# Performance work log

Hardware: AMD Instinct MI355X
Metric: run time of the kernel (lower is better)

Reference implementation:

```python
import jax, jax.numpy as jnp
import numpy as np

B, L, C = 2, 2048, 1024
H, DK = 16, 64  # multiNum, dk
EPS = 1e-5
MASK_VAL = -2**15 + 1  # matches masked_fill value in torch source


def layer_norm(x, g, b):
    mu = jnp.mean(x, axis=-1, keepdims=True)
    var = jnp.var(x, axis=-1, keepdims=True)
    return (x - mu) * jax.lax.rsqrt(var + EPS) * g + b


def setup_inputs() -> dict:
    key = jax.random.key(0)
    ks = jax.random.split(key, 12)
    s_in = 1.0 / np.sqrt(C)
    s_attn = 1.0 / np.sqrt(H * DK)
    return {
        "qx": jax.random.normal(ks[0], (B, L, C), jnp.float32),
        "kx": jax.random.normal(ks[1], (B, L, C), jnp.float32),
        "vx": jax.random.normal(ks[2], (B, L, C), jnp.float32),
        "maskPAD": jax.random.randint(ks[3], (B, L, L), 0, 2, jnp.int32),
        "ln_g": jnp.ones((C,), jnp.float32),
        "ln_b": jnp.zeros((C,), jnp.float32),
        "wq": jax.random.uniform(ks[4], (C, H * DK), jnp.float32, -s_in, s_in),
        "bq": jax.random.uniform(ks[5], (H * DK,), jnp.float32, -s_in, s_in),
        "wk": jax.random.uniform(ks[6], (C, H * DK), jnp.float32, -s_in, s_in),
        "bk": jax.random.uniform(ks[7], (H * DK,), jnp.float32, -s_in, s_in),
        "wv": jax.random.uniform(ks[8], (C, H * DK), jnp.float32, -s_in, s_in),
        "bv": jax.random.uniform(ks[9], (H * DK,), jnp.float32, -s_in, s_in),
        "wo": jax.random.uniform(ks[10], (H * DK, C), jnp.float32, -s_attn, s_attn),
        "bo": jax.random.uniform(ks[11], (C,), jnp.float32, -s_attn, s_attn),
    }


def reference(qx, kx, vx, maskPAD, ln_g, ln_b, wq, bq, wk, bk, wv, bv, wo, bo):
    # PreLN with shared LayerNorm params across q/k/v (as in source)
    qn = layer_norm(qx, ln_g, ln_b)
    kn = layer_norm(kx, ln_g, ln_b)
    vn = layer_norm(vx, ln_g, ln_b)
    # project and split heads: [B, H, L, DK]
    q = (qn @ wq + bq).reshape(B, L, H, DK).transpose(0, 2, 1, 3)
    k = (kn @ wk + bk).reshape(B, L, H, DK).transpose(0, 2, 1, 3)
    v = (vn @ wv + bv).reshape(B, L, H, DK).transpose(0, 2, 1, 3)
    scores = jnp.einsum("bhqd,bhkd->bhqk", q, k) / np.sqrt(DK).astype(np.float32)
    scores = jnp.where((maskPAD == 0)[:, None, :, :], jnp.float32(MASK_VAL), scores)
    alpha = jax.nn.softmax(scores, axis=-1)
    z = jnp.einsum("bhqk,bhkd->bhqd", alpha, v)
    z = z.transpose(0, 2, 1, 3).reshape(B, L, H * DK)
    return z @ wo + bo
```

## Files before the change

### kernel.cpp

```cpp
#include <hip/hip_runtime.h>
#include <hip/hip_bf16.h>

#define B_ 2
#define L_ 2048
#define C_ 1024
#define H_ 16
#define DK_ 64
#define M_ (B_*L_)
#define MASK_VALF (-32767.0f)
#define LOG2E 1.44269504088896f

typedef __attribute__((ext_vector_type(8))) short bf16x8;
typedef __attribute__((ext_vector_type(4))) float f32x4;
typedef __attribute__((ext_vector_type(4))) unsigned uint4v;

static __device__ __forceinline__ short f2bf(float f) {
    __hip_bfloat16 h = __float2bfloat16(f);
    return *reinterpret_cast<short*>(&h);
}

static __device__ __forceinline__ float exp2_raw(float x) {
    float r;
    asm("v_exp_f32 %0, %1" : "=v"(r) : "v"(x));
    return r;
}
static __device__ __forceinline__ unsigned cvt_pk_bf16(float lo, float hi) {
    unsigned r;
    asm("v_cvt_pk_bf16_f32 %0, %1, %2" : "=v"(r) : "v"(lo), "v"(hi));
    return r;
}

__global__ __launch_bounds__(256) void prep_kernel(
    const float* __restrict__ qx, const float* __restrict__ kx, const float* __restrict__ vx,
    const float* __restrict__ g, const float* __restrict__ bias,
    short* __restrict__ qn, short* __restrict__ kn, short* __restrict__ vn,
    const float* __restrict__ wq, const float* __restrict__ wk,
    const float* __restrict__ wv, const float* __restrict__ wo,
    short* __restrict__ wqt, short* __restrict__ wkt,
    short* __restrict__ wvt, short* __restrict__ wot,
    const int* __restrict__ mask, unsigned long long* __restrict__ bits)
{
    const int bid = blockIdx.x;
    const int t = threadIdx.x;

    if (bid < 3*M_) {
        const int row = bid & (M_ - 1);
        const int which = bid >> 12;
        const float* src = (which == 0) ? qx : (which == 1) ? kx : vx;
        short* dst = (which == 0) ? qn : (which == 1) ? kn : vn;
        src += (size_t)row * C_;
        dst += (size_t)row * C_;
        float4 xv = reinterpret_cast<const float4*>(src)[t];
        float s  = xv.x + xv.y + xv.z + xv.w;
        float s2 = xv.x*xv.x + xv.y*xv.y + xv.z*xv.z + xv.w*xv.w;
        #pragma unroll
        for (int off = 32; off > 0; off >>= 1) {
            s  += __shfl_down(s, off);
            s2 += __shfl_down(s2, off);
        }
        __shared__ float red[8];
        const int wid = t >> 6, lane = t & 63;
        if (lane == 0) { red[wid] = s; red[4 + wid] = s2; }
        __syncthreads();
        const float ts  = red[0] + red[1] + red[2] + red[3];
        const float ts2 = red[4] + red[5] + red[6] + red[7];
        const float mu  = ts * (1.0f / C_);
        const float var = ts2 * (1.0f / C_) - mu * mu;
        const float rs  = rsqrtf(var + 1e-5f);
        float4 gv = reinterpret_cast<const float4*>(g)[t];
        float4 bv = reinterpret_cast<const float4*>(bias)[t];
        short4 o;
        o.x = f2bf((xv.x - mu) * rs * gv.x + bv.x);
        o.y = f2bf((xv.y - mu) * rs * gv.y + bv.y);
        o.z = f2bf((xv.z - mu) * rs * gv.z + bv.z);
        o.w = f2bf((xv.w - mu) * rs * gv.w + bv.w);
        reinterpret_cast<short4*>(dst)[t] = o;
    } else if (bid < 3*M_ + 4096) {
        const int b2 = bid - 3*M_;
        const int mz = b2 >> 10;
        const int bx = b2 & 31, by = (b2 >> 5) & 31;
        const float* w = (mz==0)?wq:(mz==1)?wk:(mz==2)?wv:wo;
        short* wt = (mz==0)?wqt:(mz==1)?wkt:(mz==2)?wvt:wot;
        __shared__ float tile[32][33];
        const int tx = t & 31, ty = t >> 5;
        const int k0 = bx * 32, n0 = by * 32;
        #pragma unroll
        for (int r = 0; r < 4; r++) {
            const int k = k0 + ty + r*8;
            tile[ty + r*8][tx] = w[(size_t)k * 1024 + n0 + tx];
        }
        __syncthreads();
        #pragma unroll
        for (int r = 0; r < 4; r++) {
            const int n = n0 + ty + r*8;
            wt[(size_t)n * 1024 + k0 + tx] = f2bf(tile[tx][ty + r*8]);
        }
    } else {
        const int b3 = bid - (3*M_ + 4096);
        const int gw = b3 * 4 + (t >> 6);
        const int lane = t & 63;
        const int k = (gw & 31) * 64 + lane;
        const int rowq = gw >> 5;
        const int v = mask[(size_t)rowq * L_ + k];
        unsigned long long bal = __ballot(v != 0);
        if (lane == 0) bits[gw] = bal;
    }
}

__device__ __forceinline__ void gemm_core_128(
    const short* __restrict__ Abf, const short* __restrict__ Bt,
    int m0, int n0, short* lds, f32x4 (&acc)[4][4])
{
    const int t = threadIdx.x, w = t >> 6, l = t & 63;
    const int wm = w >> 1, wn = w & 1;
    const int l15 = l & 15, l4 = l >> 4;
    const int srow = t >> 2, scol = (t & 3) * 8;
    const short* aS = Abf + (size_t)(m0 + srow) * 1024 + scol;
    const short* bS = Bt  + (size_t)(n0 + srow) * 1024 + scol;
    char* lb = (char*)lds;
    const int wb = w * 1024;

    #define GSTAGE(buf, kt) do {                                                   \
        const int ko = (kt) * 32;                                                  \
        char* dst = lb + (buf)*16384;                                              \
        __builtin_amdgcn_global_load_lds(                                          \
            (const __attribute__((address_space(1))) void*)(aS + ko),              \
            (__attribute__((address_space(3))) void*)(dst + wb), 16, 0, 0);        \
        __builtin_amdgcn_global_load_lds(                                          \
            (const __attribute__((address_space(1))) void*)(aS + 64*1024 + ko),    \
            (__attribute__((address_space(3))) void*)(dst + wb + 4096), 16, 0, 0); \
        __builtin_amdgcn_global_load_lds(                                          \
            (const __attribute__((address_space(1))) void*)(bS + ko),              \
            (__attribute__((address_space(3))) void*)(dst + 8192 + wb), 16, 0, 0); \
        __builtin_amdgcn_global_load_lds(                                          \
            (const __attribute__((address_space(1))) void*)(bS + 64*1024 + ko),    \
            (__attribute__((address_space(3))) void*)(dst + 8192 + wb + 4096), 16, 0, 0); \
    } while (0)

    GSTAGE(0, 0);
    for (int kt = 0; kt < 32; ++kt) {
        __syncthreads();
        if (kt + 1 < 32) GSTAGE((kt + 1) & 1, kt + 1);
        const short* Lb = lds + (kt & 1) * 8192;
        bf16x8 af[4], bfr[4];
        #pragma unroll
        for (int fm = 0; fm < 4; fm++)
            af[fm] = *reinterpret_cast<const bf16x8*>(&Lb[(wm*64 + fm*16 + l15)*32 + l4*8]);
        #pragma unroll
        for (int fn = 0; fn < 4; fn++)
            bfr[fn] = *reinterpret_cast<const bf16x8*>(&Lb[4096 + (wn*64 + fn*16 + l15)*32 + l4*8]);
        #pragma unroll
        for (int fm = 0; fm < 4; fm++)
            #pragma unroll
            for (int fn = 0; fn < 4; fn++)
                acc[fm][fn] = __builtin_amdgcn_mfma_f32_16x16x32_bf16(af[fm], bfr[fn], acc[fm][fn], 0, 0, 0);
    }
    #undef GSTAGE
}

__global__ __launch_bounds__(256) void gemm_proj(
    const short* __restrict__ qn, const short* __restrict__ kn, const short* __restrict__ vn,
    const short* __restrict__ wqt, const short* __restrict__ wkt, const short* __restrict__ wvt,
    const float* __restrict__ bq, const float* __restrict__ bk, const float* __restrict__ bv,
    short* __restrict__ qb, short* __restrict__ kb, short* __restrict__ vtb)
{
    const int pi = blockIdx.y;
    const short* Abf = (pi==0)?qn:(pi==1)?kn:vn;
    const short* Bt  = (pi==0)?wqt:(pi==1)?wkt:wvt;
    const float* bias= (pi==0)?bq:(pi==1)?bk:bv;
    short* outp      = (pi==0)?qb:(pi==1)?kb:vtb;
    const float scale = (pi==0)?(0.125f*LOG2E):1.0f;

    __shared__ short lds[16384];
    const int bx0 = blockIdx.x;
    const int bx = (bx0 & 7) * 32 + (bx0 >> 3);
    const int m0 = (bx >> 3) * 128, n0 = (bx & 7) * 128;
    f32x4 acc[4][4] = {};
    gemm_core_128(Abf, Bt, m0, n0, lds, acc);

    const int t = threadIdx.x, w = t >> 6, l = t & 63;
    const int wm = w >> 1, wn = w & 1, l15 = l & 15, l4 = l >> 4;
    #pragma unroll
    for (int fn = 0; fn < 4; fn++) {
        const int col = n0 + wn*64 + fn*16 + l15;
        const float bsv = bias[col];
        const int h = col >> 6, dk = col & 63;
        #pragma unroll
        for (int fm = 0; fm < 4; fm++) {
            const int row0 = m0 + wm*64 + fm*16 + l4*4;
            const int bb = row0 >> 11, lr0 = row0 & (L_ - 1);
            if (pi == 2) {
                const int lrp = (lr0 & ~63) | ((fm >> 1)*32 + l4*8 + (fm & 1)*4);
                short4 s4;
                #pragma unroll
                for (int r = 0; r < 4; r++)
                    ((short*)&s4)[r] = f2bf(acc[fm][fn][r] + bsv);
                *reinterpret_cast<short4*>(
                    &outp[(((size_t)bb*H_ + h)*DK_ + dk)*L_ + lrp]) = s4;
            } else {
                #pragma unroll
                for (int r = 0; r < 4; r++) {
                    const float vvf = (acc[fm][fn][r] + bsv) * scale;
                    outp[(((size_t)bb*H_ + h)*L_ + lr0 + r)*DK_ + dk] = f2bf(vvf);
                }
            }
        }
    }
}

__global__ __launch_bounds__(256) void gemm_out_k(
    const short* __restrict__ zb, const short* __restrict__ wot,
    const float* __restrict__ bo, float* __restrict__ out)
{
    __shared__ short lds[12288];
    const int t = threadIdx.x, w = t >> 6, l = t & 63;
    const int wm = w >> 1, wn = w & 1;
    const int l15 = l & 15, l4 = l >> 4;
    const int bx0 = blockIdx.x;
    const int bx = (bx0 & 7) * 64 + (bx0 >> 3);
    const int m0 = (bx >> 3) * 64, n0 = (bx & 7) * 128;

    const int srow = l >> 2, scol = (l & 3) * 8;
    const short* aS = zb  + (size_t)(m0 + w*16 + srow) * 1024 + scol;
    const short* bS = wot + (size_t)(n0 + w*32 + srow) * 1024 + scol;
    char* lb = (char*)lds;

    f32x4 acc[2][4] = {};

    #define OSTAGE(buf, kt) do {                                                    \
        const int ko = (kt) * 32;                                                   \
        char* dst = lb + (buf)*12288;                                               \
        __builtin_amdgcn_global_load_lds(                                           \
            (const __attribute__((address_space(1))) void*)(aS + ko),               \
            (__attribute__((address_space(3))) void*)(dst + w*1024), 16, 0, 0);     \
        __builtin_amdgcn_global_load_lds(                                           \
            (const __attribute__((address_space(1))) void*)(bS + ko),               \
            (__attribute__((address_space(3))) void*)(dst + 4096 + w*2048), 16, 0, 0); \
        __builtin_amdgcn_global_load_lds(                                           \
            (const __attribute__((address_space(1))) void*)(bS + 16*1024 + ko),     \
            (__attribute__((address_space(3))) void*)(dst + 4096 + w*2048 + 1024), 16, 0, 0); \
    } while (0)

    OSTAGE(0, 0);
    for (int kt = 0; kt < 32; ++kt) {
        __syncthreads();
        if (kt + 1 < 32) OSTAGE((kt + 1) & 1, kt + 1);
        const short* Lb = lds + (kt & 1) * 6144;
        bf16x8 af[2], bfr[4];
        #pragma unroll
        for (int fm = 0; fm < 2; fm++)
            af[fm] = *reinterpret_cast<const bf16x8*>(&Lb[(wm*32 + fm*16 + l15)*32 + l4*8]);
        #pragma unroll
        for (int fn = 0; fn < 4; fn++)
            bfr[fn] = *reinterpret_cast<const bf16x8*>(&Lb[2048 + (wn*64 + fn*16 + l15)*32 + l4*8]);
        #pragma unroll
        for (int fm = 0; fm < 2; fm++)
            #pragma unroll
            for (int fn = 0; fn < 4; fn++)
                acc[fm][fn] = __builtin_amdgcn_mfma_f32_16x16x32_bf16(af[fm], bfr[fn], acc[fm][fn], 0, 0, 0);
    }
    #undef OSTAGE

    #pragma unroll
    for (int fn = 0; fn < 4; fn++) {
        const int col = n0 + wn*64 + fn*16 + l15;
        const float bsv = bo[col];
        #pragma unroll
        for (int fm = 0; fm < 2; fm++) {
            #pragma unroll
            for (int r = 0; r < 4; r++) {
                const int row = m0 + wm*32 + fm*16 + l4*4 + r;
                out[(size_t)row * C_ + col] = acc[fm][fn][r] + bsv;
            }
        }
    }
}

__global__ __launch_bounds__(512) void attn_kernel(
    const short* __restrict__ qbuf, const short* __restrict__ kbuf, const short* __restrict__ vt,
    const unsigned long long* __restrict__ mbits, short* __restrict__ zb)
{
    __shared__ char SM[65536];
    const int t = threadIdx.x, w = t >> 6, l = t & 63;
    const int l15 = l & 15, l4 = l >> 4;
    const int bid = blockIdx.x;
    const int bh = bid & 31, qb = bid >> 5;
    const int qt0 = qb * 128;
    const int b = bh >> 4, h = bh & 15;
    const size_t base  = (size_t)bh * L_ * DK_;
    const size_t vbase = (size_t)bh * DK_ * L_;

    const int q = qt0 + w*16 + l15;

    const int srow = w*8 + (l >> 3);
    const int scolb = ((l & 7) * 16) ^ ((srow & 7) << 4);

    const char* gkA = (const char*)(kbuf + base + (size_t)srow*DK_) + scolb;
    const char* gkB = gkA + 8192;
    const char* gvA = (const char*)(vt + vbase + (size_t)srow*L_) + scolb;
    const char* gvB = gvA + 128;

    char* kd0 = SM + w*1024;
    char* vd0 = SM + 8192 + w*1024;
    char* kd1 = SM + 16384 + w*1024;
    char* vd1 = SM + 16384 + 8192 + w*1024;

    const int sw = (l15 & 7) << 4;
    const char* pa = SM + l15*128 + ((l4*16) ^ sw);
    const char* pb = SM + l15*128 + ((64 + l4*16) ^ sw);

    bf16x8 qf[2];
    #pragma unroll
    for (int kk = 0; kk < 2; kk++)
        qf[kk] = *reinterpret_cast<const bf16x8*>(&qbuf[base + (size_t)q*DK_ + kk*32 + l4*8]);

    const uint2* mb32 = reinterpret_cast<const uint2*>(mbits + ((size_t)b*L_ + q) * (L_/64));

    f32x4 oacc[4];
    #pragma unroll
    for (int nt = 0; nt < 4; nt++) oacc[nt] = (f32x4){0.f, 0.f, 0.f, 0.f};
    f32x4 lacc = (f32x4){0.f, 0.f, 0.f, 0.f};

    uint4v onesu = {0x3F803F80u, 0x3F803F80u, 0x3F803F80u, 0x3F803F80u};
    const bf16x8 onesv = *reinterpret_cast<const bf16x8*>(&onesu);

    #define STAGE(kd, vd, gk, gv) do {                                               \
        __builtin_amdgcn_global_load_lds(                                            \
            (const __attribute__((address_space(1))) void*)(gk),                     \
            (__attribute__((address_space(3))) void*)(kd), 16, 0, 0);                \
        __builtin_amdgcn_global_load_lds(                                            \
            (const __attribute__((address_space(1))) void*)(gv),                     \
            (__attribute__((address_space(3))) void*)(vd), 16, 0, 0);                \
    } while (0)

    #define BODY(BOFF, mlo, mhi) do {                                               \
        f32x4 sfr[4];                                                                \
        __builtin_amdgcn_s_setprio(1);                                               \
        _Pragma("unroll")                                                            \
        for (int ct = 0; ct < 4; ct++) {                                             \
            bf16x8 kf0 = *reinterpret_cast<const bf16x8*>(pa + (BOFF) + ct*2048);    \
            bf16x8 kf1 = *reinterpret_cast<const bf16x8*>(pb + (BOFF) + ct*2048);    \
            f32x4 a = (f32x4){0.f, 0.f, 0.f, 0.f};                                   \
            a = __builtin_amdgcn_mfma_f32_16x16x32_bf16(kf0, qf[0], a, 0, 0, 0);     \
            a = __builtin_amdgcn_mfma_f32_16x16x32_bf16(kf1, qf[1], a, 0, 0, 0);     \
            sfr[ct] = a;                                                             \
        }                                                                            \
        __builtin_amdgcn_s_setprio(0);                                               \
        unsigned pu[8];                                                              \
        _Pragma("unroll")                                                            \
        for (int ct = 0; ct < 4; ct++) {                                             \
            const unsigned nib = ((((ct) < 2) ? (mlo) : (mhi))                       \
                                  >> ((ct & 1)*16 + l4*4)) & 0xFu;                   \
            float p0 = exp2_raw((nib & 1u) ? sfr[ct][0] : MASK_VALF);                \
            float p1 = exp2_raw((nib & 2u) ? sfr[ct][1] : MASK_VALF);                \
            float p2 = exp2_raw((nib & 4u) ? sfr[ct][2] : MASK_VALF);                \
            float p3 = exp2_raw((nib & 8u) ? sfr[ct][3] : MASK_VALF);                \
            pu[ct*2]     = cvt_pk_bf16(p0, p1);                                      \
            pu[ct*2 + 1] = cvt_pk_bf16(p2, p3);                                      \
        }                                                                            \
        uint4v a0v = {pu[0], pu[1], pu[2], pu[3]};                                   \
        uint4v a1v = {pu[4], pu[5], pu[6], pu[7]};                                   \
        const bf16x8 af0 = *reinterpret_cast<const bf16x8*>(&a0v);                   \
        const bf16x8 af1 = *reinterpret_cast<const bf16x8*>(&a1v);                   \
        __builtin_amdgcn_s_setprio(1);                                               \
        lacc = __builtin_amdgcn_mfma_f32_16x16x32_bf16(af0, onesv, lacc, 0, 0, 0);   \
        lacc = __builtin_amdgcn_mfma_f32_16x16x32_bf16(af1, onesv, lacc, 0, 0, 0);   \
        _Pragma("unroll")                                                            \
        for (int nt = 0; nt < 4; nt++) {                                             \
            bf16x8 vf0 = *reinterpret_cast<const bf16x8*>(pa + (BOFF) + 8192 + nt*2048); \
            bf16x8 vf1 = *reinterpret_cast<const bf16x8*>(pb + (BOFF) + 8192 + nt*2048); \
            oacc[nt] = __builtin_amdgcn_mfma_f32_16x16x32_bf16(af0, vf0, oacc[nt], 0, 0, 0); \
            oacc[nt] = __builtin_amdgcn_mfma_f32_16x16x32_bf16(af1, vf1, oacc[nt], 0, 0, 0); \
        }                                                                            \
        __builtin_amdgcn_s_setprio(0);                                               \
    } while (0)

    STAGE(kd0, vd0, gkA, gvA);
    uint2 mwv = mb32[0], mwn;

    for (int kt = 0; kt < L_/64; kt += 2) {
        __syncthreads();
        STAGE(kd1, vd1, gkB, gvB);
        mwn = mb32[kt + 1];
        BODY(0, mwv.x, mwv.y);
        mwv = mwn;
        gkA += 16384; gvA += 256;
        __syncthreads();
        if (kt + 2 < L_/64) { STAGE(kd0, vd0, gkA, gvA); mwn = mb32[kt + 2]; }
        BODY(16384, mwv.x, mwv.y);
        mwv = mwn;
        gkB += 16384; gvB += 256;
    }
    #undef STAGE
    #undef BODY

    #pragma unroll
    for (int nt = 0; nt < 4; nt++) {
        #pragma unroll
        for (int r = 0; r < 4; r++) {
            const int qg = qt0 + w*16 + l4*4 + r;
            const float ov = oacc[nt][r] / lacc[r];
            zb[((size_t)b*L_ + qg)*C_ + h*DK_ + nt*16 + l15] = f2bf(ov);
        }
    }
}

extern "C" void kernel_launch(void* const* d_in, const int* in_sizes, int n_in,
                              void* d_out, int out_size, void* d_ws, size_t ws_size,
                              hipStream_t stream)
{
    (void)in_sizes; (void)n_in; (void)out_size; (void)ws_size;
    const float* qx = (const float*)d_in[0];
    const float* kx = (const float*)d_in[1];
    const float* vx = (const float*)d_in[2];
    const int*   mp = (const int*)d_in[3];
    const float* lg = (const float*)d_in[4];
    const float* lbt= (const float*)d_in[5];
    const float* wq = (const float*)d_in[6];
    const float* bq = (const float*)d_in[7];
    const float* wk = (const float*)d_in[8];
    const float* bk = (const float*)d_in[9];
    const float* wv = (const float*)d_in[10];
    const float* bv = (const float*)d_in[11];
    const float* wo = (const float*)d_in[12];
    const float* bo = (const float*)d_in[13];
    float* out = (float*)d_out;

    short* ws0 = (short*)d_ws;
    short* qn  = ws0;
    short* kn  = qn + (size_t)M_*C_;
    short* vn  = kn + (size_t)M_*C_;
    short* wqt = vn + (size_t)M_*C_;
    short* wkt = wqt + 1024*1024;
    short* wvt = wkt + 1024*1024;
    short* wot = wvt + 1024*1024;
    short* qbuf = wot + 1024*1024;
    short* kbuf = qbuf + (size_t)M_*C_;
    short* vtb  = kbuf + (size_t)M_*C_;
    short* zbuf = vtb + (size_t)M_*C_;
    unsigned long long* mbits = (unsigned long long*)(zbuf + (size_t)M_*C_);

    hipLaunchKernelGGL(prep_kernel, dim3(3*M_ + 4096 + (B_*L_*L_/64)/4), dim3(256), 0, stream,
                       qx, kx, vx, lg, lbt, qn, kn, vn,
                       wq, wk, wv, wo, wqt, wkt, wvt, wot, mp, mbits);
    hipLaunchKernelGGL(gemm_proj, dim3(256, 3), dim3(256), 0, stream,
                       qn, kn, vn, wqt, wkt, wvt, bq, bk, bv, qbuf, kbuf, vtb);
    hipLaunchKernelGGL(attn_kernel, dim3(512), dim3(512), 0, stream,
                       qbuf, kbuf, vtb, mbits, zbuf);
    hipLaunchKernelGGL(gemm_out_k, dim3(512), dim3(256), 0, stream,
                       zbuf, wot, bo, out);
}
```

Measured before the change: 132.8 us.

## Stage two key/value tiles per barrier with wider mask loads

Restructures the attention main loop so each double-buffer half holds two 64-key K/V tiles, halving the number of workgroup barriers and prefetching a full pair ahead. The padding mask is now read as one 128-bit word per pair of tiles, and the per-lane mask shift is hoisted out of the per-block unrolled loop. This trades slightly larger in-flight staging per barrier and longer-lived registers for fewer synchronisations and more latency hiding.

```diff
diff --git a/kernel.cpp b/kernel.cpp
--- a/kernel.cpp
+++ b/kernel.cpp
@@ -295,26 +295,20 @@
     const int srow = w*8 + (l >> 3);
     const int scolb = ((l & 7) * 16) ^ ((srow & 7) << 4);
 
-    const char* gkA = (const char*)(kbuf + base + (size_t)srow*DK_) + scolb;
-    const char* gkB = gkA + 8192;
-    const char* gvA = (const char*)(vt + vbase + (size_t)srow*L_) + scolb;
-    const char* gvB = gvA + 128;
-
-    char* kd0 = SM + w*1024;
-    char* vd0 = SM + 8192 + w*1024;
-    char* kd1 = SM + 16384 + w*1024;
-    char* vd1 = SM + 16384 + 8192 + w*1024;
+    const char* gk = (const char*)(kbuf + base + (size_t)srow*DK_) + scolb;
+    const char* gv = (const char*)(vt + vbase + (size_t)srow*L_) + scolb;
 
     const int sw = (l15 & 7) << 4;
     const char* pa = SM + l15*128 + ((l4*16) ^ sw);
     const char* pb = SM + l15*128 + ((64 + l4*16) ^ sw);
+    const int l4s = l4 * 4;
 
     bf16x8 qf[2];
     #pragma unroll
     for (int kk = 0; kk < 2; kk++)
         qf[kk] = *reinterpret_cast<const bf16x8*>(&qbuf[base + (size_t)q*DK_ + kk*32 + l4*8]);
 
-    const uint2* mb32 = reinterpret_cast<const uint2*>(mbits + ((size_t)b*L_ + q) * (L_/64));
+    const uint4* mq4 = reinterpret_cast<const uint4*>(mbits + ((size_t)b*L_ + q) * (L_/64));
 
     f32x4 oacc[4];
     #pragma unroll
@@ -324,13 +318,20 @@
     uint4v onesu = {0x3F803F80u, 0x3F803F80u, 0x3F803F80u, 0x3F803F80u};
     const bf16x8 onesv = *reinterpret_cast<const bf16x8*>(&onesu);
 
-    #define STAGE(kd, vd, gk, gv) do {                                               \
+    #define STAGE2(DB) do {                                                          \
         __builtin_amdgcn_global_load_lds(                                            \
             (const __attribute__((address_space(1))) void*)(gk),                     \
-            (__attribute__((address_space(3))) void*)(kd), 16, 0, 0);                \
+            (__attribute__((address_space(3))) void*)(SM + (DB) + w*1024), 16, 0, 0); \
         __builtin_amdgcn_global_load_lds(                                            \
             (const __attribute__((address_space(1))) void*)(gv),                     \
-            (__attribute__((address_space(3))) void*)(vd), 16, 0, 0);                \
+            (__attribute__((address_space(3))) void*)(SM + (DB) + 8192 + w*1024), 16, 0, 0); \
+        __builtin_amdgcn_global_load_lds(                                            \
+            (const __attribute__((address_space(1))) void*)(gk + 8192),              \
+            (__attribute__((address_space(3))) void*)(SM + (DB) + 16384 + w*1024), 16, 0, 0); \
+        __builtin_amdgcn_global_load_lds(                                            \
+            (const __attribute__((address_space(1))) void*)(gv + 128),               \
+            (__attribute__((address_space(3))) void*)(SM + (DB) + 24576 + w*1024), 16, 0, 0); \
+        gk += 16384; gv += 256;                                                      \
     } while (0)
 
     #define BODY(BOFF, mlo, mhi) do {                                               \
@@ -346,15 +347,17 @@
             sfr[ct] = a;                                                             \
         }                                                                            \
         __builtin_amdgcn_s_setprio(0);                                               \
+        const unsigned msl = (mlo) >> l4s;                                           \
+        const unsigned msh = (mhi) >> l4s;                                           \
         unsigned pu[8];                                                              \
         _Pragma("unroll")                                                            \
         for (int ct = 0; ct < 4; ct++) {                                             \
-            const unsigned nib = ((((ct) < 2) ? (mlo) : (mhi))                       \
-                                  >> ((ct & 1)*16 + l4*4)) & 0xFu;                   \
-            float p0 = exp2_raw((nib & 1u) ? sfr[ct][0] : MASK_VALF);                \
-            float p1 = exp2_raw((nib & 2u) ? sfr[ct][1] : MASK_VALF);                \
-            float p2 = exp2_raw((nib & 4u) ? sfr[ct][2] : MASK_VALF);                \
-            float p3 = exp2_raw((nib & 8u) ? sfr[ct][3] : MASK_VALF);                \
+            const unsigned ms = (ct < 2) ? msl : msh;                                \
+            const unsigned bp = (ct & 1) * 16;                                       \
+            float p0 = exp2_raw((ms & (1u << (bp + 0))) ? sfr[ct][0] : MASK_VALF);   \
+            float p1 = exp2_raw((ms & (1u << (bp + 1))) ? sfr[ct][1] : MASK_VALF);   \
+            float p2 = exp2_raw((ms & (1u << (bp + 2))) ? sfr[ct][2] : MASK_VALF);   \
+            float p3 = exp2_raw((ms & (1u << (bp + 3))) ? sfr[ct][3] : MASK_VALF);   \
             pu[ct*2]     = cvt_pk_bf16(p0, p1);                                      \
             pu[ct*2 + 1] = cvt_pk_bf16(p2, p3);                                      \
         }                                                                            \
@@ -375,23 +378,19 @@
         __builtin_amdgcn_s_setprio(0);                                               \
     } while (0)
 
-    STAGE(kd0, vd0, gkA, gvA);
-    uint2 mwv = mb32[0], mwn;
-
-    for (int kt = 0; kt < L_/64; kt += 2) {
+    STAGE2(0);
+    uint4 mq = mq4[0], mqn;
+
+    for (int it = 0; it < 16; ++it) {
+        const int DB  = (it & 1) * 32768;
+        const int DBn = ((it + 1) & 1) * 32768;
         __syncthreads();
-        STAGE(kd1, vd1, gkB, gvB);
-        mwn = mb32[kt + 1];
-        BODY(0, mwv.x, mwv.y);
-        mwv = mwn;
-        gkA += 16384; gvA += 256;
-        __syncthreads();
-        if (kt + 2 < L_/64) { STAGE(kd0, vd0, gkA, gvA); mwn = mb32[kt + 2]; }
-        BODY(16384, mwv.x, mwv.y);
-        mwv = mwn;
-        gkB += 16384; gvB += 256;
-    }
-    #undef STAGE
+        if (it + 1 < 16) { STAGE2(DBn); mqn = mq4[it + 1]; }
+        BODY(DB,         mq.x, mq.y);
+        BODY(DB + 16384, mq.z, mq.w);
+        mq = mqn;
+    }
+    #undef STAGE2
     #undef BODY
 
     #pragma unroll
```

Result: no change. 131.6 us, median of 2 (-0.9%).
